# Optimization experiments

Hardware: AMD Instinct MI355X
Metric: run time of the kernel (lower is better)

Reference implementation:

```python
import jax, jax.numpy as jnp
import numpy as np

N_NODES = 100000
N_EDGES = 1600000
D_FEAT = 32
K = 5


def _spmm(edge_row, edge_col, edge_vals, feat):
    # y[i] = sum_{e: row[e]==i} vals[e] * feat[col[e]]  -- sparse A @ feat
    msgs = edge_vals[:, None] * feat[edge_col]  # [E, d]
    return jax.ops.segment_sum(msgs, edge_row, num_segments=N_NODES)


def setup_inputs() -> dict:
    key = jax.random.key(0)
    k1, k2, k3, k4, k5 = jax.random.split(key, 5)
    feat = jax.random.normal(k1, (N_NODES, D_FEAT), dtype=jnp.float32)
    # approximate D^{-1/2} A D^{-1/2} magnitudes: ~1/avg_degree so spectrum stays bounded
    edge_vals = jax.random.uniform(k2, (N_EDGES,), dtype=jnp.float32) * (1.0 / 16.0)
    theta = jnp.asarray([0.5, 0.4, 0.3, 0.2, 0.1], dtype=jnp.float32)
    edge_row = jax.random.randint(k3, (N_EDGES,), 0, N_NODES, dtype=jnp.int32)
    edge_col = jax.random.randint(k4, (N_EDGES,), 0, N_NODES, dtype=jnp.int32)
    return {"feat": feat, "edge_vals": edge_vals, "theta": theta,
            "edge_row": edge_row, "edge_col": edge_col}


def reference(feat, edge_vals, theta, edge_row, edge_col):
    # h = theta[0]*feat; for k>=1: feat = feat - A@feat; h += theta[k]*feat
    h = theta[0] * feat
    for k in range(1, K):
        feat = feat - _spmm(edge_row, edge_col, edge_vals, feat)
        h = h + theta[k] * feat
    return h
```

## Files before the change

### kernel.cpp

```cpp
#include <hip/hip_runtime.h>

#define N_NODES 100000
#define N_EDGES 1600000
#define D_FEAT 32

#define NWIN 512
#define RPW  ((N_NODES + NWIN - 1) / NWIN)
#define WPAD 16
#define CAP  4096

#define NOCT 8
#define OCTDIV 12500u
#define NBINS (RPW * NOCT)
#define NBPAD 2048

#define VAL_SCALE 524288.0f
#define VAL_INV   (1.0f / 524288.0f)

#define EB_BS  256
#define EB_EPT 16
#define EB_EPB (EB_BS * EB_EPT)
#define EB_NB  ((N_EDGES + EB_EPB - 1) / EB_EPB)

__device__ __forceinline__ unsigned short f2bf(float f) {
    unsigned u = __float_as_uint(f);
    unsigned r = u + 0x7fffu + ((u >> 16) & 1u);
    return (unsigned short)(r >> 16);
}
__device__ __forceinline__ float bfl(unsigned u) { return __uint_as_float(u << 16); }
__device__ __forceinline__ float bfh(unsigned u) { return __uint_as_float(u & 0xffff0000u); }


__global__ __launch_bounds__(256) void cursor_kernel(int* __restrict__ win_cursor) {
    int i = blockIdx.x * 256 + threadIdx.x;
    if (i < NWIN) win_cursor[i * WPAD] = i * CAP;
}


__global__ __launch_bounds__(EB_BS) void bucket_kernel(const int* __restrict__ row,
                                                       const int* __restrict__ col,
                                                       const float* __restrict__ vals,
                                                       int* __restrict__ win_cursor,
                                                       uint2* __restrict__ pile,
                                                       const float* __restrict__ feat,
                                                       unsigned short* __restrict__ feat16,
                                                       int n4) {
    __shared__ int wcnt[NWIN];
    __shared__ int lbase[NWIN];
    __shared__ int wbase[NWIN];
    __shared__ int ps[EB_BS];
    __shared__ uint2 stage[EB_EPB];
    int t = threadIdx.x;
    for (int i = t; i < NWIN; i += EB_BS) wcnt[i] = 0;
    __syncthreads();

    int base = blockIdx.x * EB_EPB;
    unsigned pk_[EB_EPT];
    int wr_[EB_EPT];
#pragma unroll
    for (int i = 0; i < EB_EPT; ++i) {
        int e = base + i * EB_BS + t;
        if (e < N_EDGES) {
            int r = row[e];
            int w = r / RPW;
            unsigned fx = (unsigned)__float2int_rn(vals[e] * VAL_SCALE);
            if (fx > 0x7FFFu) fx = 0x7FFFu;
            pk_[i] = ((unsigned)col[e] << 15) | fx;
            wr_[i] = (w << 8) | (r - w * RPW);
            atomicAdd(&wcnt[w], 1);
        } else wr_[i] = -1;
    }
    __syncthreads();

    int c0 = wcnt[2 * t], c1 = wcnt[2 * t + 1];
    ps[t] = c0 + c1;
    __syncthreads();
    for (int off = 1; off < EB_BS; off <<= 1) {
        int u = (t >= off) ? ps[t - off] : 0;
        __syncthreads();
        ps[t] += u;
        __syncthreads();
    }
    int pex = ps[t] - (c0 + c1);
    lbase[2 * t]     = pex;
    lbase[2 * t + 1] = pex + c0;
    __syncthreads();

    for (int i = t; i < NWIN; i += EB_BS) {
        int cw = wcnt[i];
        wbase[i] = cw ? atomicAdd(&win_cursor[i * WPAD], cw) : 0;
    }
    __syncthreads();
    for (int i = t; i < NWIN; i += EB_BS) wcnt[i] = lbase[i];
    __syncthreads();

#pragma unroll
    for (int i = 0; i < EB_EPT; ++i) {
        if (wr_[i] < 0) continue;
        int w = wr_[i] >> 8;
        int loc = atomicAdd(&wcnt[w], 1);
        stage[loc] = make_uint2(pk_[i], (unsigned)wr_[i]);
    }
    __syncthreads();

    int nedge = N_EDGES - base; if (nedge > EB_EPB) nedge = EB_EPB;
    for (int i = t; i < nedge; i += EB_BS) {
        uint2 ed = stage[i];
        int w = ed.y >> 8;
        int pos = wbase[w] + (i - lbase[w]);
        pile[pos] = make_uint2(ed.x, ed.y & 0xFFu);
    }

    for (int i = blockIdx.x * EB_BS + t; i < n4; i += EB_NB * EB_BS) {
        float4 f = reinterpret_cast<const float4*>(feat)[i];
        ushort4 o;
        o.x = f2bf(f.x); o.y = f2bf(f.y); o.z = f2bf(f.z); o.w = f2bf(f.w);
        reinterpret_cast<ushort4*>(feat16)[i] = o;
    }
}


#define GATH(qq, pp) \
    uint4 qq = *(reinterpret_cast<const uint4*>(gsrc + (size_t)((pp) >> 15) * D_FEAT) + c)
#define ACC(qq, vv) \
    a0 += (vv) * bfl(qq.x); a1 += (vv) * bfh(qq.x); a2 += (vv) * bfl(qq.y); a3 += (vv) * bfh(qq.y); \
    a4 += (vv) * bfl(qq.z); a5 += (vv) * bfh(qq.z); a6 += (vv) * bfl(qq.w); a7 += (vv) * bfh(qq.w)

__global__ __launch_bounds__(1024) void finesort_spmm1_kernel(const uint2* __restrict__ pile,
                               const int* __restrict__ win_cursor,
                               unsigned int* __restrict__ cvout,
                               int2* __restrict__ row_rng,
                               const unsigned short* __restrict__ gsrc,
                               unsigned short* __restrict__ g_out) {
    __shared__ int cnt[NBPAD];
    __shared__ int incl[NBPAD];
    __shared__ int ps[1024];
    __shared__ int rowbeg[RPW];
    __shared__ int rowend[RPW];
    __shared__ unsigned cvl[CAP];
    int w = blockIdx.x, t = threadIdx.x;
    int rbeg = w * RPW;
    int rcnt = N_NODES - rbeg;
    if (rcnt > RPW) rcnt = RPW;
    if (rcnt < 0) rcnt = 0;
    int pbeg = w * CAP;
    int pend = win_cursor[w * WPAD];
    cnt[t] = 0;
    cnt[t + 1024] = 0;
    __syncthreads();
    for (int i = pbeg + t; i < pend; i += 1024) {
        uint2 ed = pile[i];
        int oct = (int)((ed.x >> 15) / OCTDIV);
        atomicAdd(&cnt[ed.y * NOCT + oct], 1);
    }
    __syncthreads();
    int b0 = cnt[2 * t], b1 = cnt[2 * t + 1];
    ps[t] = b0 + b1;
    __syncthreads();
    for (int off = 1; off < 1024; off <<= 1) {
        int u = (t >= off) ? ps[t - off] : 0;
        __syncthreads();
        ps[t] += u;
        __syncthreads();
    }
    int pex = ps[t] - (b0 + b1);
    incl[2 * t]     = pex + b0;
    incl[2 * t + 1] = pex + b0 + b1;
    __syncthreads();
    if (t < rcnt) {
        int beg = incl[t * NOCT] - cnt[t * NOCT];
        int end = incl[t * NOCT + NOCT - 1];
        rowbeg[t] = beg;
        rowend[t] = end;
        row_rng[rbeg + t] = make_int2(pbeg + beg, pbeg + end);
    }
    __syncthreads();
    cnt[2 * t]     = incl[2 * t] - b0;
    cnt[2 * t + 1] = incl[2 * t + 1] - b1;
    __syncthreads();
    for (int i = pbeg + t; i < pend; i += 1024) {
        uint2 ed = pile[i];
        int oct = (int)((ed.x >> 15) / OCTDIV);
        int pos = atomicAdd(&cnt[ed.y * NOCT + oct], 1);
        cvl[pos] = ed.x;
        cvout[pbeg + pos] = ed.x;
    }
    __syncthreads();

    if (t < rcnt * 4) {
        int lr = t >> 2, c = t & 3;
        int e = rowbeg[lr];
        int end = rowend[lr];
        float a0=0.f,a1=0.f,a2=0.f,a3=0.f,a4=0.f,a5=0.f,a6=0.f,a7=0.f;
        for (; e + 4 <= end; e += 4) {
            unsigned p0 = cvl[e + 0], p1 = cvl[e + 1], p2 = cvl[e + 2], p3 = cvl[e + 3];
            GATH(q0, p0); GATH(q1, p1); GATH(q2, p2); GATH(q3, p3);
            float v0 = (float)(p0 & 0x7FFFu) * VAL_INV;
            float v1 = (float)(p1 & 0x7FFFu) * VAL_INV;
            float v2 = (float)(p2 & 0x7FFFu) * VAL_INV;
            float v3 = (float)(p3 & 0x7FFFu) * VAL_INV;
            ACC(q0, v0); ACC(q1, v1); ACC(q2, v2); ACC(q3, v3);
        }
        for (; e < end; ++e) {
            unsigned p = cvl[e];
            float vv = (float)(p & 0x7FFFu) * VAL_INV;
            GATH(q, p);
            ACC(q, vv);
        }
        size_t base = (size_t)(rbeg + lr) * D_FEAT + c * 8;
        uint4 qi = *reinterpret_cast<const uint4*>(gsrc + base);
        float c0=bfl(qi.x), c1=bfh(qi.x), c2=bfl(qi.y), c3=bfh(qi.y);
        float c4=bfl(qi.z), c5=bfh(qi.z), c6=bfl(qi.w), c7=bfh(qi.w);
        uint4 o;
        o.x = (unsigned)f2bf(c0 - a0) | ((unsigned)f2bf(c1 - a1) << 16);
        o.y = (unsigned)f2bf(c2 - a2) | ((unsigned)f2bf(c3 - a3) << 16);
        o.z = (unsigned)f2bf(c4 - a4) | ((unsigned)f2bf(c5 - a5) << 16);
        o.w = (unsigned)f2bf(c6 - a6) | ((unsigned)f2bf(c7 - a7) << 16);
        *reinterpret_cast<uint4*>(g_out + base) = o;
    }
}


__global__ __launch_bounds__(256) void spmm_kernel(const int2* __restrict__ row_rng,
                               const unsigned int* __restrict__ cv,
                               const unsigned short* __restrict__ gsrc,
                               unsigned short* __restrict__ g_out,
                               const unsigned short* __restrict__ f16,
                               const unsigned short* __restrict__ t1,
                               const unsigned short* __restrict__ t2,
                               const float* __restrict__ theta,
                               float* __restrict__ h,
                               int last) {
    int tid = blockIdx.x * blockDim.x + threadIdx.x;
    int r = tid >> 2;
    int c = tid & 3;
    if (r >= N_NODES) return;
    int2 rng = row_rng[r];
    int e = rng.x, end = rng.y;
    float a0=0.f,a1=0.f,a2=0.f,a3=0.f,a4=0.f,a5=0.f,a6=0.f,a7=0.f;

    for (; e + 8 <= end; e += 8) {
        unsigned p0 = cv[e + 0], p1 = cv[e + 1], p2 = cv[e + 2], p3 = cv[e + 3];
        unsigned p4 = cv[e + 4], p5 = cv[e + 5], p6 = cv[e + 6], p7 = cv[e + 7];
        GATH(q0, p0); GATH(q1, p1); GATH(q2, p2); GATH(q3, p3);
        GATH(q4, p4); GATH(q5, p5); GATH(q6, p6); GATH(q7, p7);
        float v0 = (float)(p0 & 0x7FFFu) * VAL_INV;
        float v1 = (float)(p1 & 0x7FFFu) * VAL_INV;
        float v2 = (float)(p2 & 0x7FFFu) * VAL_INV;
        float v3 = (float)(p3 & 0x7FFFu) * VAL_INV;
        float v4 = (float)(p4 & 0x7FFFu) * VAL_INV;
        float v5 = (float)(p5 & 0x7FFFu) * VAL_INV;
        float v6 = (float)(p6 & 0x7FFFu) * VAL_INV;
        float v7 = (float)(p7 & 0x7FFFu) * VAL_INV;
        ACC(q0, v0); ACC(q1, v1); ACC(q2, v2); ACC(q3, v3);
        ACC(q4, v4); ACC(q5, v5); ACC(q6, v6); ACC(q7, v7);
    }
    for (; e + 4 <= end; e += 4) {
        unsigned p0 = cv[e + 0], p1 = cv[e + 1], p2 = cv[e + 2], p3 = cv[e + 3];
        GATH(q0, p0); GATH(q1, p1); GATH(q2, p2); GATH(q3, p3);
        float v0 = (float)(p0 & 0x7FFFu) * VAL_INV;
        float v1 = (float)(p1 & 0x7FFFu) * VAL_INV;
        float v2 = (float)(p2 & 0x7FFFu) * VAL_INV;
        float v3 = (float)(p3 & 0x7FFFu) * VAL_INV;
        ACC(q0, v0); ACC(q1, v1); ACC(q2, v2); ACC(q3, v3);
    }
    for (; e < end; ++e) {
        unsigned p = cv[e];
        float v = (float)(p & 0x7FFFu) * VAL_INV;
        GATH(q, p);
        ACC(q, v);
    }

    size_t base = (size_t)r * D_FEAT + c * 8;
    uint4 qi = *reinterpret_cast<const uint4*>(gsrc + base);
    float c0=bfl(qi.x), c1=bfh(qi.x), c2=bfl(qi.y), c3=bfh(qi.y);
    float c4=bfl(qi.z), c5=bfh(qi.z), c6=bfl(qi.w), c7=bfh(qi.w);
    float n0=c0-a0, n1=c1-a1, n2=c2-a2, n3=c3-a3, n4=c4-a4, n5=c5-a5, n6=c6-a6, n7=c7-a7;

    if (!last) {
        uint4 o;
        o.x = (unsigned)f2bf(n0) | ((unsigned)f2bf(n1) << 16);
        o.y = (unsigned)f2bf(n2) | ((unsigned)f2bf(n3) << 16);
        o.z = (unsigned)f2bf(n4) | ((unsigned)f2bf(n5) << 16);
        o.w = (unsigned)f2bf(n6) | ((unsigned)f2bf(n7) << 16);
        *reinterpret_cast<uint4*>(g_out + base) = o;
    } else {
        float th0 = theta[0], th1 = theta[1], th2 = theta[2], th3 = theta[3], th4 = theta[4];
        uint4 qf = *reinterpret_cast<const uint4*>(f16 + base);
        uint4 q1 = *reinterpret_cast<const uint4*>(t1 + base);
        uint4 q2 = *reinterpret_cast<const uint4*>(t2 + base);
        float4 h0, h1;
        h0.x = th0*bfl(qf.x) + th1*bfl(q1.x) + th2*bfl(q2.x) + th3*c0 + th4*n0;
        h0.y = th0*bfh(qf.x) + th1*bfh(q1.x) + th2*bfh(q2.x) + th3*c1 + th4*n1;
        h0.z = th0*bfl(qf.y) + th1*bfl(q1.y) + th2*bfl(q2.y) + th3*c2 + th4*n2;
        h0.w = th0*bfh(qf.y) + th1*bfh(q1.y) + th2*bfh(q2.y) + th3*c3 + th4*n3;
        h1.x = th0*bfl(qf.z) + th1*bfl(q1.z) + th2*bfl(q2.z) + th3*c4 + th4*n4;
        h1.y = th0*bfh(qf.z) + th1*bfh(q1.z) + th2*bfh(q2.z) + th3*c5 + th4*n5;
        h1.z = th0*bfl(qf.w) + th1*bfl(q1.w) + th2*bfl(q2.w) + th3*c6 + th4*n6;
        h1.w = th0*bfh(qf.w) + th1*bfh(q1.w) + th2*bfh(q2.w) + th3*c7 + th4*n7;
        *reinterpret_cast<float4*>(h + base) = h0;
        *reinterpret_cast<float4*>(h + base + 4) = h1;
    }
}

extern "C" void kernel_launch(void* const* d_in, const int* in_sizes, int n_in,
                              void* d_out, int out_size, void* d_ws, size_t ws_size,
                              hipStream_t stream) {
    const float* feat  = (const float*)d_in[0];
    const float* vals  = (const float*)d_in[1];
    const float* theta = (const float*)d_in[2];
    const int*   row   = (const int*)d_in[3];
    const int*   col   = (const int*)d_in[4];
    float* h = (float*)d_out;

    char* ws = (char*)d_ws;
    size_t off = 0;
    auto alloc = [&](size_t bytes) { void* p = ws + off; off = (off + bytes + 63) & ~(size_t)63; return p; };
    unsigned short* feat16 = (unsigned short*)alloc((size_t)N_NODES * D_FEAT * sizeof(short));
    unsigned short* T1 = (unsigned short*)alloc((size_t)N_NODES * D_FEAT * sizeof(short));
    unsigned short* T2 = (unsigned short*)alloc((size_t)N_NODES * D_FEAT * sizeof(short));
    unsigned short* T3 = (unsigned short*)alloc((size_t)N_NODES * D_FEAT * sizeof(short));
    int2*  row_rng  = (int2*)alloc((size_t)N_NODES * sizeof(int2));
    int*   win_cursor = (int*)alloc((size_t)NWIN * WPAD * sizeof(int));
    uint2* pile     = (uint2*)alloc((size_t)NWIN * CAP * sizeof(uint2));
    unsigned int* cv = (unsigned int*)alloc((size_t)NWIN * CAP * sizeof(unsigned int));

    const int blk = 256;
    const int n4 = N_NODES * D_FEAT / 4;

    cursor_kernel<<<(NWIN + 255) / 256, 256, 0, stream>>>(win_cursor);
    bucket_kernel<<<EB_NB, EB_BS, 0, stream>>>(row, col, vals, win_cursor, pile, feat, feat16, n4);
    finesort_spmm1_kernel<<<NWIN, 1024, 0, stream>>>(pile, win_cursor, cv, row_rng, feat16, T1);

    const int sgrid = (N_NODES * 4 + blk - 1) / blk;
    spmm_kernel<<<sgrid, blk, 0, stream>>>(row_rng, cv, T1, T2, nullptr, nullptr, nullptr, theta, nullptr, 0);
    spmm_kernel<<<sgrid, blk, 0, stream>>>(row_rng, cv, T2, T3, nullptr, nullptr, nullptr, theta, nullptr, 0);
    spmm_kernel<<<sgrid, blk, 0, stream>>>(row_rng, cv, T3, nullptr, feat16, T1, T2, theta, h, 1);
}
```

Measured before the change: 128.3 us.

## Split edge pile into packed word and precomputed bin arrays, use wave-shuffle scans

The bucket pass now computes each edge's fine bin (row-in-window times octant plus column octant) once and stores it as a 16-bit array next to a 32-bit packed column/value array, instead of an 8-byte pair. The fine-sort kernel's counting pass reads only the 2-byte bin rather than the full pair and the division by OCTDIV, and the scatter pass reads 6 bytes per edge instead of 8. Both block-wide prefix scans are replaced by intra-wavefront shuffle scans plus a small serial combine, which removes many __syncthreads rounds. Shared staging grows slightly because it now uses two 4-byte arrays.

```diff
diff --git a/kernel.cpp b/kernel.cpp
--- a/kernel.cpp
+++ b/kernel.cpp
@@ -41,15 +41,17 @@
                                                        const int* __restrict__ col,
                                                        const float* __restrict__ vals,
                                                        int* __restrict__ win_cursor,
-                                                       uint2* __restrict__ pile,
+                                                       unsigned int* __restrict__ pilePk,
+                                                       unsigned short* __restrict__ pileBin,
                                                        const float* __restrict__ feat,
                                                        unsigned short* __restrict__ feat16,
                                                        int n4) {
     __shared__ int wcnt[NWIN];
     __shared__ int lbase[NWIN];
     __shared__ int wbase[NWIN];
-    __shared__ int ps[EB_BS];
-    __shared__ uint2 stage[EB_EPB];
+    __shared__ int wsum[4];
+    __shared__ unsigned pk_stage[EB_EPB];
+    __shared__ unsigned wr_stage[EB_EPB];
     int t = threadIdx.x;
     for (int i = t; i < NWIN; i += EB_BS) wcnt[i] = 0;
     __syncthreads();
@@ -62,28 +64,32 @@
         int e = base + i * EB_BS + t;
         if (e < N_EDGES) {
             int r = row[e];
+            int cl = col[e];
             int w = r / RPW;
             unsigned fx = (unsigned)__float2int_rn(vals[e] * VAL_SCALE);
             if (fx > 0x7FFFu) fx = 0x7FFFu;
-            pk_[i] = ((unsigned)col[e] << 15) | fx;
-            wr_[i] = (w << 8) | (r - w * RPW);
+            pk_[i] = ((unsigned)cl << 15) | fx;
+            int bin = (r - w * RPW) * NOCT + (int)((unsigned)cl / OCTDIV);
+            wr_[i] = (w << 11) | bin;
             atomicAdd(&wcnt[w], 1);
         } else wr_[i] = -1;
     }
     __syncthreads();
 
     int c0 = wcnt[2 * t], c1 = wcnt[2 * t + 1];
-    ps[t] = c0 + c1;
-    __syncthreads();
-    for (int off = 1; off < EB_BS; off <<= 1) {
-        int u = (t >= off) ? ps[t - off] : 0;
-        __syncthreads();
-        ps[t] += u;
-        __syncthreads();
-    }
-    int pex = ps[t] - (c0 + c1);
-    lbase[2 * t]     = pex;
-    lbase[2 * t + 1] = pex + c0;
+    int s = c0 + c1;
+    int lane = t & 63, wv = t >> 6;
+    for (int off = 1; off < 64; off <<= 1) {
+        int u = __shfl_up(s, off);
+        if (lane >= off) s += u;
+    }
+    if (lane == 63) wsum[wv] = s;
+    __syncthreads();
+    if (t == 0) { int a = 0; for (int i = 0; i < 4; ++i) { int x = wsum[i]; wsum[i] = a; a += x; } }
+    __syncthreads();
+    int pref = s + wsum[wv];
+    lbase[2 * t]     = pref - c0 - c1;
+    lbase[2 * t + 1] = pref - c1;
     __syncthreads();
 
     for (int i = t; i < NWIN; i += EB_BS) {
@@ -97,18 +103,20 @@
 #pragma unroll
     for (int i = 0; i < EB_EPT; ++i) {
         if (wr_[i] < 0) continue;
-        int w = wr_[i] >> 8;
+        int w = wr_[i] >> 11;
         int loc = atomicAdd(&wcnt[w], 1);
-        stage[loc] = make_uint2(pk_[i], (unsigned)wr_[i]);
+        pk_stage[loc] = pk_[i];
+        wr_stage[loc] = (unsigned)wr_[i];
     }
     __syncthreads();
 
     int nedge = N_EDGES - base; if (nedge > EB_EPB) nedge = EB_EPB;
     for (int i = t; i < nedge; i += EB_BS) {
-        uint2 ed = stage[i];
-        int w = ed.y >> 8;
+        unsigned wr = wr_stage[i];
+        int w = wr >> 11;
         int pos = wbase[w] + (i - lbase[w]);
-        pile[pos] = make_uint2(ed.x, ed.y & 0xFFu);
+        pilePk[pos] = pk_stage[i];
+        pileBin[pos] = (unsigned short)(wr & 0x7FFu);
     }
 
     for (int i = blockIdx.x * EB_BS + t; i < n4; i += EB_NB * EB_BS) {
@@ -126,7 +134,8 @@
     a0 += (vv) * bfl(qq.x); a1 += (vv) * bfh(qq.x); a2 += (vv) * bfl(qq.y); a3 += (vv) * bfh(qq.y); \
     a4 += (vv) * bfl(qq.z); a5 += (vv) * bfh(qq.z); a6 += (vv) * bfl(qq.w); a7 += (vv) * bfh(qq.w)
 
-__global__ __launch_bounds__(1024) void finesort_spmm1_kernel(const uint2* __restrict__ pile,
+__global__ __launch_bounds__(1024) void finesort_spmm1_kernel(const unsigned int* __restrict__ pilePk,
+                               const unsigned short* __restrict__ pileBin,
                                const int* __restrict__ win_cursor,
                                unsigned int* __restrict__ cvout,
                                int2* __restrict__ row_rng,
@@ -134,7 +143,7 @@
                                unsigned short* __restrict__ g_out) {
     __shared__ int cnt[NBPAD];
     __shared__ int incl[NBPAD];
-    __shared__ int ps[1024];
+    __shared__ int wsum16[16];
     __shared__ int rowbeg[RPW];
     __shared__ int rowend[RPW];
     __shared__ unsigned cvl[CAP];
@@ -145,27 +154,28 @@
     if (rcnt < 0) rcnt = 0;
     int pbeg = w * CAP;
     int pend = win_cursor[w * WPAD];
+    int n = pend - pbeg;
     cnt[t] = 0;
     cnt[t + 1024] = 0;
     __syncthreads();
-    for (int i = pbeg + t; i < pend; i += 1024) {
-        uint2 ed = pile[i];
-        int oct = (int)((ed.x >> 15) / OCTDIV);
-        atomicAdd(&cnt[ed.y * NOCT + oct], 1);
+    for (int i = t; i < n; i += 1024) {
+        atomicAdd(&cnt[pileBin[pbeg + i]], 1);
     }
     __syncthreads();
     int b0 = cnt[2 * t], b1 = cnt[2 * t + 1];
-    ps[t] = b0 + b1;
-    __syncthreads();
-    for (int off = 1; off < 1024; off <<= 1) {
-        int u = (t >= off) ? ps[t - off] : 0;
-        __syncthreads();
-        ps[t] += u;
-        __syncthreads();
-    }
-    int pex = ps[t] - (b0 + b1);
-    incl[2 * t]     = pex + b0;
-    incl[2 * t + 1] = pex + b0 + b1;
+    int s = b0 + b1;
+    int lane = t & 63, wv = t >> 6;
+    for (int off = 1; off < 64; off <<= 1) {
+        int u = __shfl_up(s, off);
+        if (lane >= off) s += u;
+    }
+    if (lane == 63) wsum16[wv] = s;
+    __syncthreads();
+    if (t == 0) { int a = 0; for (int i = 0; i < 16; ++i) { int x = wsum16[i]; wsum16[i] = a; a += x; } }
+    __syncthreads();
+    int pref = s + wsum16[wv];
+    incl[2 * t]     = pref - b1;
+    incl[2 * t + 1] = pref;
     __syncthreads();
     if (t < rcnt) {
         int beg = incl[t * NOCT] - cnt[t * NOCT];
@@ -178,12 +188,12 @@
     cnt[2 * t]     = incl[2 * t] - b0;
     cnt[2 * t + 1] = incl[2 * t + 1] - b1;
     __syncthreads();
-    for (int i = pbeg + t; i < pend; i += 1024) {
-        uint2 ed = pile[i];
-        int oct = (int)((ed.x >> 15) / OCTDIV);
-        int pos = atomicAdd(&cnt[ed.y * NOCT + oct], 1);
-        cvl[pos] = ed.x;
-        cvout[pbeg + pos] = ed.x;
+    for (int i = t; i < n; i += 1024) {
+        unsigned pk = pilePk[pbeg + i];
+        int bin = pileBin[pbeg + i];
+        int pos = atomicAdd(&cnt[bin], 1);
+        cvl[pos] = pk;
+        cvout[pbeg + pos] = pk;
     }
     __syncthreads();
 
@@ -322,15 +332,16 @@
     unsigned short* T3 = (unsigned short*)alloc((size_t)N_NODES * D_FEAT * sizeof(short));
     int2*  row_rng  = (int2*)alloc((size_t)N_NODES * sizeof(int2));
     int*   win_cursor = (int*)alloc((size_t)NWIN * WPAD * sizeof(int));
-    uint2* pile     = (uint2*)alloc((size_t)NWIN * CAP * sizeof(uint2));
+    unsigned int*   pilePk  = (unsigned int*)alloc((size_t)NWIN * CAP * sizeof(unsigned int));
+    unsigned short* pileBin = (unsigned short*)alloc((size_t)NWIN * CAP * sizeof(unsigned short));
     unsigned int* cv = (unsigned int*)alloc((size_t)NWIN * CAP * sizeof(unsigned int));
 
     const int blk = 256;
     const int n4 = N_NODES * D_FEAT / 4;
 
     cursor_kernel<<<(NWIN + 255) / 256, 256, 0, stream>>>(win_cursor);
-    bucket_kernel<<<EB_NB, EB_BS, 0, stream>>>(row, col, vals, win_cursor, pile, feat, feat16, n4);
-    finesort_spmm1_kernel<<<NWIN, 1024, 0, stream>>>(pile, win_cursor, cv, row_rng, feat16, T1);
+    bucket_kernel<<<EB_NB, EB_BS, 0, stream>>>(row, col, vals, win_cursor, pilePk, pileBin, feat, feat16, n4);
+    finesort_spmm1_kernel<<<NWIN, 1024, 0, stream>>>(pilePk, pileBin, win_cursor, cv, row_rng, feat16, T1);
 
     const int sgrid = (N_NODES * 4 + blk - 1) / blk;
     spmm_kernel<<<sgrid, blk, 0, stream>>>(row_rng, cv, T1, T2, nullptr, nullptr, nullptr, theta, nullptr, 0);
```

Measured after the change: 129.5 us. Within noise of the previous version (+0.9%).
